# Optimization experiments

Hardware: AMD Instinct MI355X
Metric: run time of the kernel (lower is better)

Reference implementation:

```python
import jax, jax.numpy as jnp
import numpy as np

B, S, H = 4, 1024, 256      # batch, num_spans, hidden
R = 65536                   # num_relations
FFN = int(2 * H * 1.5)      # 768


def setup_inputs() -> dict:
    key = jax.random.key(0)
    k1, k2, k3, k4 = jax.random.split(key, 4)
    span_reps = jax.random.normal(k1, (B, S, H), dtype=jnp.float32)
    rel_ids = jax.random.randint(k2, (B, R, 2), 0, S, dtype=jnp.int64)
    W1 = jax.random.normal(k3, (2 * H, FFN), dtype=jnp.float32) * (1.0 / np.sqrt(2 * H))
    b1 = jnp.zeros((FFN,), dtype=jnp.float32)
    W2 = jax.random.normal(k4, (FFN, H), dtype=jnp.float32) * (1.0 / np.sqrt(FFN))
    b2 = jnp.zeros((H,), dtype=jnp.float32)
    return {"span_reps": span_reps, "rel_ids": rel_ids, "W1": W1, "b1": b1, "W2": W2, "b2": b2}


def reference(span_reps, rel_ids, W1, b1, W2, b2):
    # gather head/tail span reps: (B, R, H) each
    head = jnp.take_along_axis(span_reps, rel_ids[..., 0:1], axis=1)  # via batched gather
    tail = jnp.take_along_axis(span_reps, rel_ids[..., 1:2], axis=1)
    rel = jnp.concatenate([head, tail], axis=-1)  # (B, R, 2H)
    # FFN projection: Linear -> ReLU -> (dropout: identity at eval) -> Linear
    h = jax.nn.relu(jnp.einsum('brk,kf->brf', rel, W1) + b1)
    out = jnp.einsum('brf,fh->brh', h, W2) + b2  # (B, R, H)
    return out
```

## Files before the change

### kernel.cpp

```cpp
#include <hip/hip_runtime.h>

#define NB 4
#define NS 1024
#define NH 256
#define NR 65536
#define NF 768
#define NK 512

typedef __attribute__((ext_vector_type(8))) short bf16x8;
typedef __attribute__((ext_vector_type(4))) float f32x4;

static __device__ __forceinline__ unsigned short f2bf(float f) {
  unsigned int u = __builtin_bit_cast(unsigned int, f);
  u += 0x7FFFu + ((u >> 16) & 1u);
  return (unsigned short)(u >> 16);
}

static __device__ __forceinline__ unsigned cvt_pk(float a, float b) {
  unsigned r;
  asm("v_cvt_pk_bf16_f32 %0, %1, %2" : "=v"(r) : "v"(a), "v"(b));
  return r;
}

#define BARRIER()                                            \
  do {                                                       \
    asm volatile("s_waitcnt lgkmcnt(0)" ::: "memory");       \
    __builtin_amdgcn_s_barrier();                            \
    asm volatile("" ::: "memory");                           \
  } while (0)

__global__ void prep_all(const float* __restrict__ w1, const float* __restrict__ w2,
                         const int* __restrict__ ids,
                         unsigned short* __restrict__ w1f,
                         unsigned short* __restrict__ w2f,
                         int* __restrict__ flag) {
  int bid = blockIdx.x;
  if (bid < 192) {
    int t = bid * 256 + threadIdx.x;
    int l = t & 63;
    int kk = (t >> 6) & 15;
    int half = (t >> 10) & 1;
    int w = (t >> 11) & 3;
    int c = t >> 13;
    int row = c * 128 + w * 32 + half * 16 + (l & 15);
    int k0 = kk * 32 + (l >> 4) * 8;
    uint4 pk;
    unsigned short v[8];
#pragma unroll
    for (int j = 0; j < 8; ++j) v[j] = f2bf(w1[(size_t)(k0 + j) * NF + row]);
    pk.x = v[0] | ((unsigned)v[1] << 16);
    pk.y = v[2] | ((unsigned)v[3] << 16);
    pk.z = v[4] | ((unsigned)v[5] << 16);
    pk.w = v[6] | ((unsigned)v[7] << 16);
    *(uint4*)(w1f + (size_t)t * 8) = pk;
  } else if (bid < 288) {
    int t = (bid - 192) * 256 + threadIdx.x;
    int l = t & 63;
    int kq = (t >> 6) & 3;
    int rest = t >> 8;
    int c = rest % 6;
    int wn = rest / 6;
    int nj = wn & 3;
    int w = wn >> 2;
    int row = w * 64 + nj * 16 + (l & 15);
    int k = c * 128 + kq * 32 + (l >> 4) * 8;
    uint4 pk;
    unsigned short v[8];
#pragma unroll
    for (int j = 0; j < 8; ++j) v[j] = f2bf(w2[(size_t)(k + j) * NH + row]);
    pk.x = v[0] | ((unsigned)v[1] << 16);
    pk.y = v[2] | ((unsigned)v[3] << 16);
    pk.z = v[4] | ((unsigned)v[5] << 16);
    pk.w = v[6] | ((unsigned)v[7] << 16);
    *(uint4*)(w2f + (size_t)t * 8) = pk;
  } else {
    __shared__ int anynz;
    if (threadIdx.x == 0) anynz = 0;
    __syncthreads();
    int acc = 0;
    for (int i = threadIdx.x; i < 8192; i += 256) acc |= ids[2 * i + 1];
    if (acc != 0) atomicOr(&anynz, 1);
    __syncthreads();
    if (threadIdx.x == 0) flag[0] = (anynz == 0) ? 1 : 0;
  }
}

__global__ __launch_bounds__(256, 2)
void fused_relffn(const float* __restrict__ span, const int* __restrict__ ids,
                  const float* __restrict__ b1, const float* __restrict__ b2,
                  const unsigned short* __restrict__ w1f,
                  const unsigned short* __restrict__ w2f,
                  const int* __restrict__ flagp, float* __restrict__ out) {
  __shared__ __align__(16) unsigned short As[64 * 512];
  __shared__ __align__(16) unsigned short Hs[64 * 128];

  const int tid = threadIdx.x;
  const int blk = blockIdx.x;
  const int bb = blk >> 10;
  const int r0 = (blk & 1023) << 6;
  const int lane = tid & 63;
  const int w = tid >> 6;
  const int l15 = lane & 15;
  const int lq = lane >> 4;
  const int is64 = flagp[0];

  const unsigned short* w1base = w1f + w * 16384 + lane * 8;
  const unsigned short* w2base = w2f + w * 49152 + lane * 8;

  {
    const long pair0 = ((long)bb * NR + r0) * 2;
    int idv[16];
#pragma unroll
    for (int j = 0; j < 16; ++j) {
      int g = tid + j * 256;
      int row = g >> 6;
      int kc = g & 63;
      long pidx = pair0 + row * 2 + (kc >> 5);
      idv[j] = is64 ? ids[pidx * 2] : ids[pidx];
    }
#pragma unroll
    for (int j = 0; j < 16; ++j) {
      int g = tid + j * 256;
      int row = g >> 6;
      int kc = g & 63;
      const float* src = span + ((size_t)bb * NS + idv[j]) * NH + (kc & 31) * 8;
      float4 v0 = *(const float4*)src;
      float4 v1 = *(const float4*)(src + 4);
      uint4 pk;
      pk.x = cvt_pk(v0.x, v0.y);
      pk.y = cvt_pk(v0.z, v0.w);
      pk.z = cvt_pk(v1.x, v1.y);
      pk.w = cvt_pk(v1.z, v1.w);
      int idx = row * 512 + ((kc * 8) ^ ((row & 7) << 3));
      *(uint4*)&As[idx] = pk;
    }
  }
  BARRIER();

  f32x4 acc2[4][4];
#pragma unroll
  for (int mi = 0; mi < 4; ++mi)
#pragma unroll
    for (int nj = 0; nj < 4; ++nj) {
      f32x4 z = {0.f, 0.f, 0.f, 0.f};
      acc2[mi][nj] = z;
    }

  for (int cp = 0; cp < 3; ++cp) {
    const int ca = cp * 2, cb = ca + 1;
    const unsigned short* wpa = w1base + ca * 65536;
    const unsigned short* wpb = w1base + cb * 65536;

    f32x4 acc1a[4][2], acc1b[4][2];
#pragma unroll
    for (int mi = 0; mi < 4; ++mi)
#pragma unroll
      for (int ni = 0; ni < 2; ++ni) {
        f32x4 z = {0.f, 0.f, 0.f, 0.f};
        acc1a[mi][ni] = z;
        acc1b[mi][ni] = z;
      }

    bf16x8 wfa[2][2], wfb[2][2];
#pragma unroll
    for (int d = 0; d < 2; ++d) {
      wfa[d][0] = *(const bf16x8*)(wpa + d * 512);
      wfa[d][1] = *(const bf16x8*)(wpa + 8192 + d * 512);
      wfb[d][0] = *(const bf16x8*)(wpb + d * 512);
      wfb[d][1] = *(const bf16x8*)(wpb + 8192 + d * 512);
    }
    bf16x8 afp[2][4];
#pragma unroll
    for (int mi = 0; mi < 4; ++mi) {
      int row = mi * 16 + l15;
      afp[0][mi] = *(const bf16x8*)&As[row * 512 + ((lq * 8) ^ ((row & 7) << 3))];
    }

#pragma unroll
    for (int kk = 0; kk < 16; ++kk) {
      const int cur = kk & 1;
      if (kk < 15) {
#pragma unroll
        for (int mi = 0; mi < 4; ++mi) {
          int row = mi * 16 + l15;
          int kidx = (kk + 1) * 32 + lq * 8;
          afp[cur ^ 1][mi] = *(const bf16x8*)&As[row * 512 + (kidx ^ ((row & 7) << 3))];
        }
      }
      bf16x8 ca0 = wfa[cur][0], ca1 = wfa[cur][1];
      bf16x8 cb0 = wfb[cur][0], cb1 = wfb[cur][1];
      if (kk < 14) {
        wfa[cur][0] = *(const bf16x8*)(wpa + (kk + 2) * 512);
        wfa[cur][1] = *(const bf16x8*)(wpa + 8192 + (kk + 2) * 512);
        wfb[cur][0] = *(const bf16x8*)(wpb + (kk + 2) * 512);
        wfb[cur][1] = *(const bf16x8*)(wpb + 8192 + (kk + 2) * 512);
      }
      __builtin_amdgcn_s_setprio(1);
#pragma unroll
      for (int mi = 0; mi < 4; ++mi) {
        bf16x8 a = afp[cur][mi];
        acc1a[mi][0] = __builtin_amdgcn_mfma_f32_16x16x32_bf16(ca0, a, acc1a[mi][0], 0, 0, 0);
        acc1a[mi][1] = __builtin_amdgcn_mfma_f32_16x16x32_bf16(ca1, a, acc1a[mi][1], 0, 0, 0);
        acc1b[mi][0] = __builtin_amdgcn_mfma_f32_16x16x32_bf16(cb0, a, acc1b[mi][0], 0, 0, 0);
        acc1b[mi][1] = __builtin_amdgcn_mfma_f32_16x16x32_bf16(cb1, a, acc1b[mi][1], 0, 0, 0);
      }
      __builtin_amdgcn_s_setprio(0);
    }

#pragma unroll
    for (int half = 0; half < 2; ++half) {
      const int c = half ? cb : ca;
      BARRIER();
#pragma unroll
      for (int ni = 0; ni < 2; ++ni) {
        int n0 = c * 128 + w * 32 + ni * 16 + lq * 4;
        float4 bv = *(const float4*)(b1 + n0);
#pragma unroll
        for (int mi = 0; mi < 4; ++mi) {
          f32x4 a = half ? acc1b[mi][ni] : acc1a[mi][ni];
          float x0 = fmaxf(a[0] + bv.x, 0.0f);
          float x1 = fmaxf(a[1] + bv.y, 0.0f);
          float x2 = fmaxf(a[2] + bv.z, 0.0f);
          float x3 = fmaxf(a[3] + bv.w, 0.0f);
          int m = mi * 16 + l15;
          int nl0 = w * 32 + ni * 16 + lq * 4;
          uint2 pk;
          pk.x = cvt_pk(x0, x1);
          pk.y = cvt_pk(x2, x3);
          *(uint2*)&Hs[m * 128 + (nl0 ^ ((m & 7) << 3))] = pk;
        }
      }
      BARRIER();
      const unsigned short* w2p = w2base + c * 2048;
#pragma unroll
      for (int kq = 0; kq < 4; ++kq) {
        bf16x8 vf[4];
#pragma unroll
        for (int nj = 0; nj < 4; ++nj)
          vf[nj] = *(const bf16x8*)(w2p + nj * 12288 + kq * 512);
        bf16x8 hf[4];
#pragma unroll
        for (int mi = 0; mi < 4; ++mi) {
          int row = mi * 16 + l15;
          int kidx = kq * 32 + lq * 8;
          hf[mi] = *(const bf16x8*)&Hs[row * 128 + (kidx ^ ((row & 7) << 3))];
        }
        __builtin_amdgcn_s_setprio(1);
#pragma unroll
        for (int mi = 0; mi < 4; ++mi)
#pragma unroll
          for (int nj = 0; nj < 4; ++nj)
            acc2[mi][nj] = __builtin_amdgcn_mfma_f32_16x16x32_bf16(vf[nj], hf[mi], acc2[mi][nj], 0, 0, 0);
        __builtin_amdgcn_s_setprio(0);
      }
    }
  }

#pragma unroll
  for (int nj = 0; nj < 4; ++nj) {
    int n0 = w * 64 + nj * 16 + lq * 4;
    float4 bv = *(const float4*)(b2 + n0);
#pragma unroll
    for (int mi = 0; mi < 4; ++mi) {
      int m = mi * 16 + l15;
      f32x4 a = acc2[mi][nj];
      float4 o;
      o.x = a[0] + bv.x; o.y = a[1] + bv.y; o.z = a[2] + bv.z; o.w = a[3] + bv.w;
      *(float4*)(out + ((size_t)bb * NR + r0 + m) * NH + n0) = o;
    }
  }
}

extern "C" void kernel_launch(void* const* d_in, const int* in_sizes, int n_in,
                              void* d_out, int out_size, void* d_ws, size_t ws_size,
                              hipStream_t stream) {
  const float* span = (const float*)d_in[0];
  const int* ids = (const int*)d_in[1];
  const float* W1 = (const float*)d_in[2];
  const float* b1 = (const float*)d_in[3];
  const float* W2 = (const float*)d_in[4];
  const float* b2 = (const float*)d_in[5];
  float* out = (float*)d_out;

  char* ws = (char*)d_ws;
  int* flag = (int*)ws;
  unsigned short* w1f = (unsigned short*)(ws + 64);
  unsigned short* w2f = (unsigned short*)(ws + 64 + NF * NK * 2);

  prep_all<<<289, 256, 0, stream>>>(W1, W2, ids, w1f, w2f, flag);
  fused_relffn<<<4096, 256, 0, stream>>>(span, ids, b1, b2, w1f, w2f, flag, out);
}
```

Baseline: 307.0 us.

## Switch both GEMMs from 16x16x32 to 32x32x16 bf16 MFMA tiles

Replaces the 16x16x32 MFMA tiling in both FFN GEMMs with 32x32x16 MFMA tiles. The prepacked W1/W2 fragment layouts, LDS fragment reads, and epilogue index mapping all change to match. The second GEMM now double-buffers its W2 fragments and H tile reads across k-steps, and W2 loads are issued before the barrier. Larger MFMA tiles cut the instruction count and the number of fragment loads per FLOP, in exchange for different register pressure and different LDS access patterns.

```diff
diff --git a/kernel.cpp b/kernel.cpp
--- a/kernel.cpp
+++ b/kernel.cpp
@@ -9,6 +9,7 @@
 
 typedef __attribute__((ext_vector_type(8))) short bf16x8;
 typedef __attribute__((ext_vector_type(4))) float f32x4;
+typedef __attribute__((ext_vector_type(16))) float f32x16;
 
 static __device__ __forceinline__ unsigned short f2bf(float f) {
   unsigned int u = __builtin_bit_cast(unsigned int, f);
@@ -38,16 +39,15 @@
   if (bid < 192) {
     int t = bid * 256 + threadIdx.x;
     int l = t & 63;
-    int kk = (t >> 6) & 15;
-    int half = (t >> 10) & 1;
+    int s = (t >> 6) & 31;
     int w = (t >> 11) & 3;
     int c = t >> 13;
-    int row = c * 128 + w * 32 + half * 16 + (l & 15);
-    int k0 = kk * 32 + (l >> 4) * 8;
+    int n1 = c * 128 + w * 32 + (l & 31);
+    int k0 = s * 16 + (l >> 5) * 8;
     uint4 pk;
     unsigned short v[8];
 #pragma unroll
-    for (int j = 0; j < 8; ++j) v[j] = f2bf(w1[(size_t)(k0 + j) * NF + row]);
+    for (int j = 0; j < 8; ++j) v[j] = f2bf(w1[(size_t)(k0 + j) * NF + n1]);
     pk.x = v[0] | ((unsigned)v[1] << 16);
     pk.y = v[2] | ((unsigned)v[3] << 16);
     pk.z = v[4] | ((unsigned)v[5] << 16);
@@ -56,18 +56,18 @@
   } else if (bid < 288) {
     int t = (bid - 192) * 256 + threadIdx.x;
     int l = t & 63;
-    int kq = (t >> 6) & 3;
-    int rest = t >> 8;
+    int ks = (t >> 6) & 7;
+    int rest = t >> 9;
     int c = rest % 6;
     int wn = rest / 6;
-    int nj = wn & 3;
-    int w = wn >> 2;
-    int row = w * 64 + nj * 16 + (l & 15);
-    int k = c * 128 + kq * 32 + (l >> 4) * 8;
+    int nt = wn & 1;
+    int w = wn >> 1;
+    int n2 = w * 64 + nt * 32 + (l & 31);
+    int k2 = c * 128 + ks * 16 + (l >> 5) * 8;
     uint4 pk;
     unsigned short v[8];
 #pragma unroll
-    for (int j = 0; j < 8; ++j) v[j] = f2bf(w2[(size_t)(k + j) * NH + row]);
+    for (int j = 0; j < 8; ++j) v[j] = f2bf(w2[(size_t)(k2 + j) * NH + n2]);
     pk.x = v[0] | ((unsigned)v[1] << 16);
     pk.y = v[2] | ((unsigned)v[3] << 16);
     pk.z = v[4] | ((unsigned)v[5] << 16);
@@ -100,8 +100,8 @@
   const int r0 = (blk & 1023) << 6;
   const int lane = tid & 63;
   const int w = tid >> 6;
-  const int l15 = lane & 15;
-  const int lq = lane >> 4;
+  const int l31 = lane & 31;
+  const int l5 = lane >> 5;
   const int is64 = flagp[0];
 
   const unsigned short* w1base = w1f + w * 16384 + lane * 8;
@@ -137,72 +137,58 @@
   }
   BARRIER();
 
-  f32x4 acc2[4][4];
-#pragma unroll
-  for (int mi = 0; mi < 4; ++mi)
-#pragma unroll
-    for (int nj = 0; nj < 4; ++nj) {
-      f32x4 z = {0.f, 0.f, 0.f, 0.f};
-      acc2[mi][nj] = z;
-    }
+  f32x16 acc2[2][2];
+#pragma unroll
+  for (int mi = 0; mi < 2; ++mi)
+#pragma unroll
+    for (int nt = 0; nt < 2; ++nt)
+#pragma unroll
+      for (int r = 0; r < 16; ++r) acc2[mi][nt][r] = 0.f;
 
   for (int cp = 0; cp < 3; ++cp) {
     const int ca = cp * 2, cb = ca + 1;
     const unsigned short* wpa = w1base + ca * 65536;
     const unsigned short* wpb = w1base + cb * 65536;
 
-    f32x4 acc1a[4][2], acc1b[4][2];
-#pragma unroll
-    for (int mi = 0; mi < 4; ++mi)
-#pragma unroll
-      for (int ni = 0; ni < 2; ++ni) {
-        f32x4 z = {0.f, 0.f, 0.f, 0.f};
-        acc1a[mi][ni] = z;
-        acc1b[mi][ni] = z;
-      }
-
-    bf16x8 wfa[2][2], wfb[2][2];
-#pragma unroll
-    for (int d = 0; d < 2; ++d) {
-      wfa[d][0] = *(const bf16x8*)(wpa + d * 512);
-      wfa[d][1] = *(const bf16x8*)(wpa + 8192 + d * 512);
-      wfb[d][0] = *(const bf16x8*)(wpb + d * 512);
-      wfb[d][1] = *(const bf16x8*)(wpb + 8192 + d * 512);
-    }
-    bf16x8 afp[2][4];
-#pragma unroll
-    for (int mi = 0; mi < 4; ++mi) {
-      int row = mi * 16 + l15;
-      afp[0][mi] = *(const bf16x8*)&As[row * 512 + ((lq * 8) ^ ((row & 7) << 3))];
-    }
-
-#pragma unroll
-    for (int kk = 0; kk < 16; ++kk) {
-      const int cur = kk & 1;
-      if (kk < 15) {
-#pragma unroll
-        for (int mi = 0; mi < 4; ++mi) {
-          int row = mi * 16 + l15;
-          int kidx = (kk + 1) * 32 + lq * 8;
-          afp[cur ^ 1][mi] = *(const bf16x8*)&As[row * 512 + (kidx ^ ((row & 7) << 3))];
-        }
-      }
-      bf16x8 ca0 = wfa[cur][0], ca1 = wfa[cur][1];
-      bf16x8 cb0 = wfb[cur][0], cb1 = wfb[cur][1];
-      if (kk < 14) {
-        wfa[cur][0] = *(const bf16x8*)(wpa + (kk + 2) * 512);
-        wfa[cur][1] = *(const bf16x8*)(wpa + 8192 + (kk + 2) * 512);
-        wfb[cur][0] = *(const bf16x8*)(wpb + (kk + 2) * 512);
-        wfb[cur][1] = *(const bf16x8*)(wpb + 8192 + (kk + 2) * 512);
+    f32x16 acc1a[2], acc1b[2];
+#pragma unroll
+    for (int mi = 0; mi < 2; ++mi)
+#pragma unroll
+      for (int r = 0; r < 16; ++r) { acc1a[mi][r] = 0.f; acc1b[mi][r] = 0.f; }
+
+    bf16x8 wfa[2], wfb[2];
+    wfa[0] = *(const bf16x8*)(wpa);
+    wfa[1] = *(const bf16x8*)(wpa + 512);
+    wfb[0] = *(const bf16x8*)(wpb);
+    wfb[1] = *(const bf16x8*)(wpb + 512);
+    bf16x8 afp[2][2];
+#pragma unroll
+    for (int mi = 0; mi < 2; ++mi) {
+      int row = mi * 32 + l31;
+      afp[0][mi] = *(const bf16x8*)&As[row * 512 + ((l5 * 8) ^ ((row & 7) << 3))];
+    }
+
+#pragma unroll
+    for (int s = 0; s < 32; ++s) {
+      const int cur = s & 1;
+      if (s < 31) {
+#pragma unroll
+        for (int mi = 0; mi < 2; ++mi) {
+          int row = mi * 32 + l31;
+          int col = (s + 1) * 16 + l5 * 8;
+          afp[cur ^ 1][mi] = *(const bf16x8*)&As[row * 512 + (col ^ ((row & 7) << 3))];
+        }
+      }
+      bf16x8 ca_ = wfa[cur], cb_ = wfb[cur];
+      if (s < 30) {
+        wfa[cur] = *(const bf16x8*)(wpa + (s + 2) * 512);
+        wfb[cur] = *(const bf16x8*)(wpb + (s + 2) * 512);
       }
       __builtin_amdgcn_s_setprio(1);
 #pragma unroll
-      for (int mi = 0; mi < 4; ++mi) {
-        bf16x8 a = afp[cur][mi];
-        acc1a[mi][0] = __builtin_amdgcn_mfma_f32_16x16x32_bf16(ca0, a, acc1a[mi][0], 0, 0, 0);
-        acc1a[mi][1] = __builtin_amdgcn_mfma_f32_16x16x32_bf16(ca1, a, acc1a[mi][1], 0, 0, 0);
-        acc1b[mi][0] = __builtin_amdgcn_mfma_f32_16x16x32_bf16(cb0, a, acc1b[mi][0], 0, 0, 0);
-        acc1b[mi][1] = __builtin_amdgcn_mfma_f32_16x16x32_bf16(cb1, a, acc1b[mi][1], 0, 0, 0);
+      for (int mi = 0; mi < 2; ++mi) {
+        acc1a[mi] = __builtin_amdgcn_mfma_f32_32x32x16_bf16(ca_, afp[cur][mi], acc1a[mi], 0, 0, 0);
+        acc1b[mi] = __builtin_amdgcn_mfma_f32_32x32x16_bf16(cb_, afp[cur][mi], acc1b[mi], 0, 0, 0);
       }
       __builtin_amdgcn_s_setprio(0);
     }
@@ -210,63 +196,85 @@
 #pragma unroll
     for (int half = 0; half < 2; ++half) {
       const int c = half ? cb : ca;
+      const unsigned short* w2p = w2base + c * 4096;
+      bf16x8 vf2[2][2];
+#pragma unroll
+      for (int nt = 0; nt < 2; ++nt) {
+        vf2[0][nt] = *(const bf16x8*)(w2p + nt * 24576);
+        vf2[1][nt] = *(const bf16x8*)(w2p + nt * 24576 + 512);
+      }
+
       BARRIER();
 #pragma unroll
-      for (int ni = 0; ni < 2; ++ni) {
-        int n0 = c * 128 + w * 32 + ni * 16 + lq * 4;
-        float4 bv = *(const float4*)(b1 + n0);
-#pragma unroll
-        for (int mi = 0; mi < 4; ++mi) {
-          f32x4 a = half ? acc1b[mi][ni] : acc1a[mi][ni];
-          float x0 = fmaxf(a[0] + bv.x, 0.0f);
-          float x1 = fmaxf(a[1] + bv.y, 0.0f);
-          float x2 = fmaxf(a[2] + bv.z, 0.0f);
-          float x3 = fmaxf(a[3] + bv.w, 0.0f);
-          int m = mi * 16 + l15;
-          int nl0 = w * 32 + ni * 16 + lq * 4;
+      for (int mi = 0; mi < 2; ++mi) {
+        const int m = mi * 32 + l31;
+#pragma unroll
+        for (int g = 0; g < 4; ++g) {
+          int nl = w * 32 + g * 8 + 4 * l5;
+          float4 bv = *(const float4*)(b1 + c * 128 + nl);
+          f32x16 a = half ? acc1b[mi] : acc1a[mi];
+          float x0 = fmaxf(a[4 * g + 0] + bv.x, 0.0f);
+          float x1 = fmaxf(a[4 * g + 1] + bv.y, 0.0f);
+          float x2 = fmaxf(a[4 * g + 2] + bv.z, 0.0f);
+          float x3 = fmaxf(a[4 * g + 3] + bv.w, 0.0f);
           uint2 pk;
           pk.x = cvt_pk(x0, x1);
           pk.y = cvt_pk(x2, x3);
-          *(uint2*)&Hs[m * 128 + (nl0 ^ ((m & 7) << 3))] = pk;
+          *(uint2*)&Hs[m * 128 + (nl ^ ((m & 7) << 3))] = pk;
         }
       }
       BARRIER();
-      const unsigned short* w2p = w2base + c * 2048;
-#pragma unroll
-      for (int kq = 0; kq < 4; ++kq) {
-        bf16x8 vf[4];
-#pragma unroll
-        for (int nj = 0; nj < 4; ++nj)
-          vf[nj] = *(const bf16x8*)(w2p + nj * 12288 + kq * 512);
-        bf16x8 hf[4];
-#pragma unroll
-        for (int mi = 0; mi < 4; ++mi) {
-          int row = mi * 16 + l15;
-          int kidx = kq * 32 + lq * 8;
-          hf[mi] = *(const bf16x8*)&Hs[row * 128 + (kidx ^ ((row & 7) << 3))];
+      bf16x8 hfp[2][2];
+#pragma unroll
+      for (int mi = 0; mi < 2; ++mi) {
+        int row = mi * 32 + l31;
+        hfp[0][mi] = *(const bf16x8*)&Hs[row * 128 + ((l5 * 8) ^ ((row & 7) << 3))];
+      }
+#pragma unroll
+      for (int ks = 0; ks < 8; ++ks) {
+        const int cur = ks & 1;
+        if (ks < 7) {
+#pragma unroll
+          for (int mi = 0; mi < 2; ++mi) {
+            int row = mi * 32 + l31;
+            int col = (ks + 1) * 16 + l5 * 8;
+            hfp[cur ^ 1][mi] = *(const bf16x8*)&Hs[row * 128 + (col ^ ((row & 7) << 3))];
+          }
+        }
+        bf16x8 v0 = vf2[cur][0], v1 = vf2[cur][1];
+        if (ks < 6) {
+          vf2[cur][0] = *(const bf16x8*)(w2p + (ks + 2) * 512);
+          vf2[cur][1] = *(const bf16x8*)(w2p + 24576 + (ks + 2) * 512);
         }
         __builtin_amdgcn_s_setprio(1);
 #pragma unroll
-        for (int mi = 0; mi < 4; ++mi)
-#pragma unroll
-          for (int nj = 0; nj < 4; ++nj)
-            acc2[mi][nj] = __builtin_amdgcn_mfma_f32_16x16x32_bf16(vf[nj], hf[mi], acc2[mi][nj], 0, 0, 0);
+        for (int mi = 0; mi < 2; ++mi) {
+          acc2[mi][0] = __builtin_amdgcn_mfma_f32_32x32x16_bf16(v0, hfp[cur][mi], acc2[mi][0], 0, 0, 0);
+          acc2[mi][1] = __builtin_amdgcn_mfma_f32_32x32x16_bf16(v1, hfp[cur][mi], acc2[mi][1], 0, 0, 0);
+        }
         __builtin_amdgcn_s_setprio(0);
       }
     }
   }
 
 #pragma unroll
-  for (int nj = 0; nj < 4; ++nj) {
-    int n0 = w * 64 + nj * 16 + lq * 4;
-    float4 bv = *(const float4*)(b2 + n0);
-#pragma unroll
-    for (int mi = 0; mi < 4; ++mi) {
-      int m = mi * 16 + l15;
-      f32x4 a = acc2[mi][nj];
-      float4 o;
-      o.x = a[0] + bv.x; o.y = a[1] + bv.y; o.z = a[2] + bv.z; o.w = a[3] + bv.w;
-      *(float4*)(out + ((size_t)bb * NR + r0 + m) * NH + n0) = o;
+  for (int mi = 0; mi < 2; ++mi) {
+    const int m = mi * 32 + l31;
+    float* orow = out + ((size_t)bb * NR + r0 + m) * NH;
+#pragma unroll
+    for (int nt = 0; nt < 2; ++nt) {
+#pragma unroll
+      for (int g = 0; g < 4; ++g) {
+        int n0 = w * 64 + nt * 32 + g * 8 + 4 * l5;
+        float4 bv = *(const float4*)(b2 + n0);
+        f32x16 a = acc2[mi][nt];
+        float4 o;
+        o.x = a[4 * g + 0] + bv.x;
+        o.y = a[4 * g + 1] + bv.y;
+        o.z = a[4 * g + 2] + bv.z;
+        o.w = a[4 * g + 3] + bv.w;
+        *(float4*)(orow + n0) = o;
+      }
     }
   }
 }
```

Result: slower. 326.5 us (+6.4%).

## Software-pipeline GEMM2 of previous chunk into GEMM1 loop and swizzle block order

Applied to the files above, without the earlier changes.

Restructures the FFN loop so each of the six 128-wide hidden chunks is processed one at a time. The second GEMM for the previous chunk is interleaved with the first GEMM of the current chunk, and a tail loop handles the last chunk. Register prefetch of W1 and A fragments is deepened to 3-4 stages, and W1 fragments for the next chunk are preloaded before the gather. The block index is also remapped so that consecutive workgroups spread across batches and row tiles. This is meant to hide the serialized GEMM2 phase and its LDS and global load latency behind GEMM1 MFMAs, at the cost of more live registers and possible spills under launch_bounds(256,2).

```diff
diff --git a/kernel.cpp b/kernel.cpp
--- a/kernel.cpp
+++ b/kernel.cpp
@@ -95,7 +95,8 @@
   __shared__ __align__(16) unsigned short Hs[64 * 128];
 
   const int tid = threadIdx.x;
-  const int blk = blockIdx.x;
+  const int blk0 = blockIdx.x;
+  const int blk = (blk0 & 7) * 512 + (blk0 >> 3);
   const int bb = blk >> 10;
   const int r0 = (blk & 1023) << 6;
   const int lane = tid & 63;
@@ -106,6 +107,13 @@
 
   const unsigned short* w1base = w1f + w * 16384 + lane * 8;
   const unsigned short* w2base = w2f + w * 49152 + lane * 8;
+
+  bf16x8 wfc[4][2];
+#pragma unroll
+  for (int s = 0; s < 3; ++s) {
+    wfc[s][0] = *(const bf16x8*)(w1base + s * 512);
+    wfc[s][1] = *(const bf16x8*)(w1base + 8192 + s * 512);
+  }
 
   {
     const long pair0 = ((long)bb * NR + r0) * 2;
@@ -146,113 +154,147 @@
       acc2[mi][nj] = z;
     }
 
-  for (int cp = 0; cp < 3; ++cp) {
-    const int ca = cp * 2, cb = ca + 1;
-    const unsigned short* wpa = w1base + ca * 65536;
-    const unsigned short* wpb = w1base + cb * 65536;
-
-    f32x4 acc1a[4][2], acc1b[4][2];
+  bf16x8 afp[3][4];
+  bf16x8 hfq[3];
+  bf16x8 vfp[2][4];
+
+  for (int c = 0; c < 6; ++c) {
+    const unsigned short* wp = w1base + c * 65536;
+    const unsigned short* w2prev = w2base + (c - 1) * 2048;
+
+    f32x4 acc1[4][2];
 #pragma unroll
     for (int mi = 0; mi < 4; ++mi)
 #pragma unroll
       for (int ni = 0; ni < 2; ++ni) {
         f32x4 z = {0.f, 0.f, 0.f, 0.f};
-        acc1a[mi][ni] = z;
-        acc1b[mi][ni] = z;
-      }
-
-    bf16x8 wfa[2][2], wfb[2][2];
-#pragma unroll
-    for (int d = 0; d < 2; ++d) {
-      wfa[d][0] = *(const bf16x8*)(wpa + d * 512);
-      wfa[d][1] = *(const bf16x8*)(wpa + 8192 + d * 512);
-      wfb[d][0] = *(const bf16x8*)(wpb + d * 512);
-      wfb[d][1] = *(const bf16x8*)(wpb + 8192 + d * 512);
-    }
-    bf16x8 afp[2][4];
-#pragma unroll
-    for (int mi = 0; mi < 4; ++mi) {
-      int row = mi * 16 + l15;
-      afp[0][mi] = *(const bf16x8*)&As[row * 512 + ((lq * 8) ^ ((row & 7) << 3))];
+        acc1[mi][ni] = z;
+      }
+
+#pragma unroll
+    for (int s = 0; s < 2; ++s)
+#pragma unroll
+      for (int mi = 0; mi < 4; ++mi) {
+        int row = mi * 16 + l15;
+        int kidx = s * 32 + lq * 8;
+        afp[s][mi] = *(const bf16x8*)&As[row * 512 + (kidx ^ ((row & 7) << 3))];
+      }
+    if (c > 0) {
+#pragma unroll
+      for (int s = 0; s < 2; ++s) {
+        int row = (s & 3) * 16 + l15;
+        int kidx = lq * 8;
+        hfq[s] = *(const bf16x8*)&Hs[row * 128 + (kidx ^ ((row & 7) << 3))];
+      }
     }
 
 #pragma unroll
     for (int kk = 0; kk < 16; ++kk) {
-      const int cur = kk & 1;
-      if (kk < 15) {
+      if (kk < 14) {
 #pragma unroll
         for (int mi = 0; mi < 4; ++mi) {
           int row = mi * 16 + l15;
-          int kidx = (kk + 1) * 32 + lq * 8;
-          afp[cur ^ 1][mi] = *(const bf16x8*)&As[row * 512 + (kidx ^ ((row & 7) << 3))];
+          int kidx = (kk + 2) * 32 + lq * 8;
+          afp[(kk + 2) % 3][mi] = *(const bf16x8*)&As[row * 512 + (kidx ^ ((row & 7) << 3))];
         }
       }
-      bf16x8 ca0 = wfa[cur][0], ca1 = wfa[cur][1];
-      bf16x8 cb0 = wfb[cur][0], cb1 = wfb[cur][1];
+      if (c > 0 && kk < 14) {
+        int row = ((kk + 2) & 3) * 16 + l15;
+        int kidx = ((kk + 2) >> 2) * 32 + lq * 8;
+        hfq[(kk + 2) % 3] = *(const bf16x8*)&Hs[row * 128 + (kidx ^ ((row & 7) << 3))];
+      }
+      if (kk < 13) {
+        wfc[(kk + 3) & 3][0] = *(const bf16x8*)(wp + (kk + 3) * 512);
+        wfc[(kk + 3) & 3][1] = *(const bf16x8*)(wp + 8192 + (kk + 3) * 512);
+      }
+      if (c > 0 && kk < 12) {
+        int kq1 = (kk >> 2) + 1;
+        vfp[kq1 & 1][kk & 3] = *(const bf16x8*)(w2prev + (kk & 3) * 12288 + kq1 * 512);
+      }
+
+      __builtin_amdgcn_s_setprio(1);
+#pragma unroll
+      for (int mi = 0; mi < 4; ++mi) {
+        bf16x8 a = afp[kk % 3][mi];
+        acc1[mi][0] = __builtin_amdgcn_mfma_f32_16x16x32_bf16(wfc[kk & 3][0], a, acc1[mi][0], 0, 0, 0);
+        acc1[mi][1] = __builtin_amdgcn_mfma_f32_16x16x32_bf16(wfc[kk & 3][1], a, acc1[mi][1], 0, 0, 0);
+      }
+      if (c > 0) {
+        const int mi2 = kk & 3;
+        const int kq = kk >> 2;
+        bf16x8 h = hfq[kk % 3];
+#pragma unroll
+        for (int nj = 0; nj < 4; ++nj)
+          acc2[mi2][nj] = __builtin_amdgcn_mfma_f32_16x16x32_bf16(vfp[kq & 1][nj], h, acc2[mi2][nj], 0, 0, 0);
+      }
+      __builtin_amdgcn_s_setprio(0);
+    }
+
+    if (c < 5) {
+      const unsigned short* np = w1base + (c + 1) * 65536;
+#pragma unroll
+      for (int s = 0; s < 3; ++s) {
+        wfc[s][0] = *(const bf16x8*)(np + s * 512);
+        wfc[s][1] = *(const bf16x8*)(np + 8192 + s * 512);
+      }
+    }
+    {
+      const unsigned short* w2cur = w2base + c * 2048;
+#pragma unroll
+      for (int nj = 0; nj < 4; ++nj)
+        vfp[0][nj] = *(const bf16x8*)(w2cur + nj * 12288);
+    }
+
+    BARRIER();
+#pragma unroll
+    for (int ni = 0; ni < 2; ++ni) {
+      int n0 = c * 128 + w * 32 + ni * 16 + lq * 4;
+      float4 bv = *(const float4*)(b1 + n0);
+#pragma unroll
+      for (int mi = 0; mi < 4; ++mi) {
+        f32x4 a = acc1[mi][ni];
+        float x0 = fmaxf(a[0] + bv.x, 0.0f);
+        float x1 = fmaxf(a[1] + bv.y, 0.0f);
+        float x2 = fmaxf(a[2] + bv.z, 0.0f);
+        float x3 = fmaxf(a[3] + bv.w, 0.0f);
+        int m = mi * 16 + l15;
+        int nl0 = w * 32 + ni * 16 + lq * 4;
+        uint2 pk;
+        pk.x = cvt_pk(x0, x1);
+        pk.y = cvt_pk(x2, x3);
+        *(uint2*)&Hs[m * 128 + (nl0 ^ ((m & 7) << 3))] = pk;
+      }
+    }
+    BARRIER();
+  }
+
+  {
+    const unsigned short* w2p = w2base + 5 * 2048;
+#pragma unroll
+    for (int s = 0; s < 2; ++s) {
+      int row = (s & 3) * 16 + l15;
+      int kidx = lq * 8;
+      hfq[s] = *(const bf16x8*)&Hs[row * 128 + (kidx ^ ((row & 7) << 3))];
+    }
+#pragma unroll
+    for (int kk = 0; kk < 16; ++kk) {
       if (kk < 14) {
-        wfa[cur][0] = *(const bf16x8*)(wpa + (kk + 2) * 512);
-        wfa[cur][1] = *(const bf16x8*)(wpa + 8192 + (kk + 2) * 512);
-        wfb[cur][0] = *(const bf16x8*)(wpb + (kk + 2) * 512);
-        wfb[cur][1] = *(const bf16x8*)(wpb + 8192 + (kk + 2) * 512);
-      }
+        int row = ((kk + 2) & 3) * 16 + l15;
+        int kidx = ((kk + 2) >> 2) * 32 + lq * 8;
+        hfq[(kk + 2) % 3] = *(const bf16x8*)&Hs[row * 128 + (kidx ^ ((row & 7) << 3))];
+      }
+      if (kk < 12) {
+        int kq1 = (kk >> 2) + 1;
+        vfp[kq1 & 1][kk & 3] = *(const bf16x8*)(w2p + (kk & 3) * 12288 + kq1 * 512);
+      }
+      const int mi2 = kk & 3;
+      const int kq = kk >> 2;
+      bf16x8 h = hfq[kk % 3];
       __builtin_amdgcn_s_setprio(1);
 #pragma unroll
-      for (int mi = 0; mi < 4; ++mi) {
-        bf16x8 a = afp[cur][mi];
-        acc1a[mi][0] = __builtin_amdgcn_mfma_f32_16x16x32_bf16(ca0, a, acc1a[mi][0], 0, 0, 0);
-        acc1a[mi][1] = __builtin_amdgcn_mfma_f32_16x16x32_bf16(ca1, a, acc1a[mi][1], 0, 0, 0);
-        acc1b[mi][0] = __builtin_amdgcn_mfma_f32_16x16x32_bf16(cb0, a, acc1b[mi][0], 0, 0, 0);
-        acc1b[mi][1] = __builtin_amdgcn_mfma_f32_16x16x32_bf16(cb1, a, acc1b[mi][1], 0, 0, 0);
-      }
+      for (int nj = 0; nj < 4; ++nj)
+        acc2[mi2][nj] = __builtin_amdgcn_mfma_f32_16x16x32_bf16(vfp[kq & 1][nj], h, acc2[mi2][nj], 0, 0, 0);
       __builtin_amdgcn_s_setprio(0);
-    }
-
-#pragma unroll
-    for (int half = 0; half < 2; ++half) {
-      const int c = half ? cb : ca;
-      BARRIER();
-#pragma unroll
-      for (int ni = 0; ni < 2; ++ni) {
-        int n0 = c * 128 + w * 32 + ni * 16 + lq * 4;
-        float4 bv = *(const float4*)(b1 + n0);
-#pragma unroll
-        for (int mi = 0; mi < 4; ++mi) {
-          f32x4 a = half ? acc1b[mi][ni] : acc1a[mi][ni];
-          float x0 = fmaxf(a[0] + bv.x, 0.0f);
-          float x1 = fmaxf(a[1] + bv.y, 0.0f);
-          float x2 = fmaxf(a[2] + bv.z, 0.0f);
-          float x3 = fmaxf(a[3] + bv.w, 0.0f);
-          int m = mi * 16 + l15;
-          int nl0 = w * 32 + ni * 16 + lq * 4;
-          uint2 pk;
-          pk.x = cvt_pk(x0, x1);
-          pk.y = cvt_pk(x2, x3);
-          *(uint2*)&Hs[m * 128 + (nl0 ^ ((m & 7) << 3))] = pk;
-        }
-      }
-      BARRIER();
-      const unsigned short* w2p = w2base + c * 2048;
-#pragma unroll
-      for (int kq = 0; kq < 4; ++kq) {
-        bf16x8 vf[4];
-#pragma unroll
-        for (int nj = 0; nj < 4; ++nj)
-          vf[nj] = *(const bf16x8*)(w2p + nj * 12288 + kq * 512);
-        bf16x8 hf[4];
-#pragma unroll
-        for (int mi = 0; mi < 4; ++mi) {
-          int row = mi * 16 + l15;
-          int kidx = kq * 32 + lq * 8;
-          hf[mi] = *(const bf16x8*)&Hs[row * 128 + (kidx ^ ((row & 7) << 3))];
-        }
-        __builtin_amdgcn_s_setprio(1);
-#pragma unroll
-        for (int mi = 0; mi < 4; ++mi)
-#pragma unroll
-          for (int nj = 0; nj < 4; ++nj)
-            acc2[mi][nj] = __builtin_amdgcn_mfma_f32_16x16x32_bf16(vf[nj], hf[mi], acc2[mi][nj], 0, 0, 0);
-        __builtin_amdgcn_s_setprio(0);
-      }
     }
   }
 
```

Result: slower. 363.8 us (+18.5%).

## Double-buffer the hidden tile and overlap ReLU packing with second-GEMM MFMAs

Applied to the files above, without the earlier changes.

Splits the 128-column hidden chunk into two 64-column halves stored in a double-buffered LDS tile. Half of the waves pack bias+ReLU results into one buffer while all waves run second-GEMM MFMAs on the other. W2 fragments are prefetched one stage ahead. The first W1 fragments for the next chunk pair are also issued before the epilogue, so they are in flight across the chunk-pair boundary. This hides LDS write and global-load latency behind matrix work, at the cost of more live registers and a more intricate barrier schedule.

```diff
diff --git a/kernel.cpp b/kernel.cpp
--- a/kernel.cpp
+++ b/kernel.cpp
@@ -92,7 +92,7 @@
                   const unsigned short* __restrict__ w2f,
                   const int* __restrict__ flagp, float* __restrict__ out) {
   __shared__ __align__(16) unsigned short As[64 * 512];
-  __shared__ __align__(16) unsigned short Hs[64 * 128];
+  __shared__ __align__(16) unsigned short Hb[2][64 * 64];
 
   const int tid = threadIdx.x;
   const int blk = blockIdx.x;
@@ -102,10 +102,21 @@
   const int w = tid >> 6;
   const int l15 = lane & 15;
   const int lq = lane >> 4;
+  const int half = w >> 1;
+  const int wl = w & 1;
   const int is64 = flagp[0];
 
   const unsigned short* w1base = w1f + w * 16384 + lane * 8;
   const unsigned short* w2base = w2f + w * 49152 + lane * 8;
+
+  bf16x8 wfa[2][2], wfb[2][2];
+#pragma unroll
+  for (int d = 0; d < 2; ++d) {
+    wfa[d][0] = *(const bf16x8*)(w1base + d * 512);
+    wfa[d][1] = *(const bf16x8*)(w1base + 8192 + d * 512);
+    wfb[d][0] = *(const bf16x8*)(w1base + 65536 + d * 512);
+    wfb[d][1] = *(const bf16x8*)(w1base + 65536 + 8192 + d * 512);
+  }
 
   {
     const long pair0 = ((long)bb * NR + r0) * 2;
@@ -146,6 +157,60 @@
       acc2[mi][nj] = z;
     }
 
+  bf16x8 vf[2][4];
+
+  auto VFLOAD = [&](int c_, int q0_) {
+    const unsigned short* p = w2base + c_ * 2048;
+#pragma unroll
+    for (int kqL = 0; kqL < 2; ++kqL)
+#pragma unroll
+      for (int nj = 0; nj < 4; ++nj)
+        vf[kqL][nj] = *(const bf16x8*)(p + (q0_ + kqL) * 512 + nj * 12288);
+  };
+
+  auto G2READ = [&](bf16x8 hf[2][4], const unsigned short* bufp) {
+#pragma unroll
+    for (int mi = 0; mi < 4; ++mi) {
+      int row = mi * 16 + l15;
+      int sz = (row & 7) << 3;
+      hf[0][mi] = *(const bf16x8*)&bufp[row * 64 + ((lq * 8) ^ sz)];
+      hf[1][mi] = *(const bf16x8*)&bufp[row * 64 + ((32 + lq * 8) ^ sz)];
+    }
+  };
+  auto G2MFMA = [&](bf16x8 hf[2][4]) {
+    __builtin_amdgcn_s_setprio(1);
+#pragma unroll
+    for (int kqL = 0; kqL < 2; ++kqL)
+#pragma unroll
+      for (int mi = 0; mi < 4; ++mi)
+#pragma unroll
+        for (int nj = 0; nj < 4; ++nj)
+          acc2[mi][nj] = __builtin_amdgcn_mfma_f32_16x16x32_bf16(vf[kqL][nj], hf[kqL][mi], acc2[mi][nj], 0, 0, 0);
+    __builtin_amdgcn_s_setprio(0);
+  };
+
+  auto PACK = [&](const f32x4 acc1[4][2], int c_, unsigned short* bufp) {
+#pragma unroll
+    for (int ni = 0; ni < 2; ++ni) {
+      int n0 = c_ * 128 + w * 32 + ni * 16 + lq * 4;
+      float4 bv = *(const float4*)(b1 + n0);
+#pragma unroll
+      for (int mi = 0; mi < 4; ++mi) {
+        f32x4 a = acc1[mi][ni];
+        float x0 = fmaxf(a[0] + bv.x, 0.0f);
+        float x1 = fmaxf(a[1] + bv.y, 0.0f);
+        float x2 = fmaxf(a[2] + bv.z, 0.0f);
+        float x3 = fmaxf(a[3] + bv.w, 0.0f);
+        int m = mi * 16 + l15;
+        int nl = wl * 32 + ni * 16 + lq * 4;
+        uint2 pk;
+        pk.x = cvt_pk(x0, x1);
+        pk.y = cvt_pk(x2, x3);
+        *(uint2*)&bufp[m * 64 + (nl ^ ((m & 7) << 3))] = pk;
+      }
+    }
+  };
+
   for (int cp = 0; cp < 3; ++cp) {
     const int ca = cp * 2, cb = ca + 1;
     const unsigned short* wpa = w1base + ca * 65536;
@@ -160,22 +225,12 @@
         acc1a[mi][ni] = z;
         acc1b[mi][ni] = z;
       }
-
-    bf16x8 wfa[2][2], wfb[2][2];
-#pragma unroll
-    for (int d = 0; d < 2; ++d) {
-      wfa[d][0] = *(const bf16x8*)(wpa + d * 512);
-      wfa[d][1] = *(const bf16x8*)(wpa + 8192 + d * 512);
-      wfb[d][0] = *(const bf16x8*)(wpb + d * 512);
-      wfb[d][1] = *(const bf16x8*)(wpb + 8192 + d * 512);
-    }
     bf16x8 afp[2][4];
 #pragma unroll
     for (int mi = 0; mi < 4; ++mi) {
       int row = mi * 16 + l15;
       afp[0][mi] = *(const bf16x8*)&As[row * 512 + ((lq * 8) ^ ((row & 7) << 3))];
     }
-
 #pragma unroll
     for (int kk = 0; kk < 16; ++kk) {
       const int cur = kk & 1;
@@ -207,53 +262,62 @@
       __builtin_amdgcn_s_setprio(0);
     }
 
-#pragma unroll
-    for (int half = 0; half < 2; ++half) {
-      const int c = half ? cb : ca;
-      BARRIER();
-#pragma unroll
-      for (int ni = 0; ni < 2; ++ni) {
-        int n0 = c * 128 + w * 32 + ni * 16 + lq * 4;
-        float4 bv = *(const float4*)(b1 + n0);
-#pragma unroll
-        for (int mi = 0; mi < 4; ++mi) {
-          f32x4 a = half ? acc1b[mi][ni] : acc1a[mi][ni];
-          float x0 = fmaxf(a[0] + bv.x, 0.0f);
-          float x1 = fmaxf(a[1] + bv.y, 0.0f);
-          float x2 = fmaxf(a[2] + bv.z, 0.0f);
-          float x3 = fmaxf(a[3] + bv.w, 0.0f);
-          int m = mi * 16 + l15;
-          int nl0 = w * 32 + ni * 16 + lq * 4;
-          uint2 pk;
-          pk.x = cvt_pk(x0, x1);
-          pk.y = cvt_pk(x2, x3);
-          *(uint2*)&Hs[m * 128 + (nl0 ^ ((m & 7) << 3))] = pk;
-        }
-      }
-      BARRIER();
-      const unsigned short* w2p = w2base + c * 2048;
-#pragma unroll
-      for (int kq = 0; kq < 4; ++kq) {
-        bf16x8 vf[4];
-#pragma unroll
-        for (int nj = 0; nj < 4; ++nj)
-          vf[nj] = *(const bf16x8*)(w2p + nj * 12288 + kq * 512);
-        bf16x8 hf[4];
-#pragma unroll
-        for (int mi = 0; mi < 4; ++mi) {
-          int row = mi * 16 + l15;
-          int kidx = kq * 32 + lq * 8;
-          hf[mi] = *(const bf16x8*)&Hs[row * 128 + (kidx ^ ((row & 7) << 3))];
-        }
-        __builtin_amdgcn_s_setprio(1);
-#pragma unroll
-        for (int mi = 0; mi < 4; ++mi)
-#pragma unroll
-          for (int nj = 0; nj < 4; ++nj)
-            acc2[mi][nj] = __builtin_amdgcn_mfma_f32_16x16x32_bf16(vf[nj], hf[mi], acc2[mi][nj], 0, 0, 0);
-        __builtin_amdgcn_s_setprio(0);
-      }
-    }
+    if (cp < 2) {
+      const unsigned short* npa = w1base + (ca + 2) * 65536;
+      const unsigned short* npb = w1base + (cb + 2) * 65536;
+#pragma unroll
+      for (int d = 0; d < 2; ++d) {
+        wfa[d][0] = *(const bf16x8*)(npa + d * 512);
+        wfa[d][1] = *(const bf16x8*)(npa + 8192 + d * 512);
+        wfb[d][0] = *(const bf16x8*)(npb + d * 512);
+        wfb[d][1] = *(const bf16x8*)(npb + 8192 + d * 512);
+      }
+    }
+
+    if (cp > 0) {
+      VFLOAD(ca - 1, 2);
+      bf16x8 hf[2][4];
+      G2READ(hf, &Hb[1][0]);
+      if (half == 0) PACK(acc1a, ca, &Hb[0][0]);
+      G2MFMA(hf);
+    } else {
+      if (half == 0) PACK(acc1a, ca, &Hb[0][0]);
+    }
+    VFLOAD(ca, 0);
+    BARRIER();
+
+    {
+      bf16x8 hf[2][4];
+      G2READ(hf, &Hb[0][0]);
+      if (half == 1) PACK(acc1a, ca, &Hb[1][0]);
+      G2MFMA(hf);
+    }
+    VFLOAD(ca, 2);
+    BARRIER();
+
+    {
+      bf16x8 hf[2][4];
+      G2READ(hf, &Hb[1][0]);
+      if (half == 0) PACK(acc1b, cb, &Hb[0][0]);
+      G2MFMA(hf);
+    }
+    VFLOAD(cb, 0);
+    BARRIER();
+
+    {
+      bf16x8 hf[2][4];
+      G2READ(hf, &Hb[0][0]);
+      if (half == 1) PACK(acc1b, cb, &Hb[1][0]);
+      G2MFMA(hf);
+    }
+    if (cp == 2) VFLOAD(5, 2);
+    BARRIER();
+  }
+
+  {
+    bf16x8 hf[2][4];
+    G2READ(hf, &Hb[1][0]);
+    G2MFMA(hf);
   }
 
 #pragma unroll
```

Measured after the change: 397.9 us. +29.6%, slower.
